# Kernel optimization log

Hardware: AMD Instinct MI355X
Metric: run time of the kernel (lower is better)

## Reference

```python
import jax, jax.numpy as jnp
import numpy as np

DIM = 128
N_IN = DIM * 2 * 6          # 1536
H = N_IN // 2               # 768
W2 = N_IN * 2               # 3072
B, T = 256, 64


def _lrelu(a):
    return jnp.where(a >= 0, a, 0.1 * a)


def _lin(x, w, b):
    # torch Linear: y = x @ w.T + b, w is [out, in]
    return x @ w.T + b


def setup_inputs() -> dict:
    key = jax.random.key(0)
    ks = jax.random.split(key, 32)
    s = 0.02
    d = {
        'x': jax.random.normal(ks[0], (B, T, N_IN), jnp.float32),
        'h0r': jax.random.normal(ks[1], (B, H), jnp.float32) / 100.0,
        'h0i': jax.random.normal(ks[2], (B, H), jnp.float32) / 100.0,
        'Ur_w': jax.random.normal(ks[3], (H, H)) * s, 'Ur_b': jnp.zeros((H,)),
        'Ui_w': jax.random.normal(ks[4], (H, H)) * s, 'Ui_b': jnp.zeros((H,)),
        'Wr_w': jax.random.normal(ks[5], (H, H)) * s, 'Wr_b': jnp.zeros((H,)),
        'Wi_w': jax.random.normal(ks[6], (H, H)) * s, 'Wi_b': jnp.zeros((H,)),
        'l1r_w': jax.random.normal(ks[7], (W2, H)) * s, 'l1r_b': jnp.zeros((W2,)),
        'l1i_w': jax.random.normal(ks[8], (W2, H)) * s, 'l1i_b': jnp.zeros((W2,)),
        'l2r_w': jax.random.normal(ks[9], (W2, W2)) * s, 'l2r_b': jnp.zeros((W2,)),
        'l2i_w': jax.random.normal(ks[10], (W2, W2)) * s, 'l2i_b': jnp.zeros((W2,)),
        'l3r_w': jax.random.normal(ks[11], (W2, W2)) * s, 'l3r_b': jnp.zeros((W2,)),
        'l3i_w': jax.random.normal(ks[12], (W2, W2)) * s, 'l3i_b': jnp.zeros((W2,)),
        'l5_w': jax.random.normal(ks[13], (1, 2 * W2)) * s, 'l5_b': jnp.zeros((1,)),
    }
    return {k: v.astype(jnp.float32) for k, v in d.items()}


def reference(x, h0r, h0i, Ur_w, Ur_b, Ui_w, Ui_b, Wr_w, Wr_b, Wi_w, Wi_b,
              l1r_w, l1r_b, l1i_w, l1i_b, l2r_w, l2r_b, l2i_w, l2i_b,
              l3r_w, l3r_b, l3i_w, l3i_b, l5_w, l5_b):
    xr = x[:, :, :H]            # [B,T,H]
    xi = x[:, :, -H:]
    # Precompute the input projections for every timestep (batched GEMM).
    ur_xr = jnp.einsum('bti,oi->bto', xr, Ur_w) + Ur_b
    ur_xi = jnp.einsum('bti,oi->bto', xi, Ur_w) + Ur_b
    ui_xr = jnp.einsum('bti,oi->bto', xr, Ui_w) + Ui_b
    ui_xi = jnp.einsum('bti,oi->bto', xi, Ui_w) + Ui_b
    # scan over time: [T,B,H]
    seq = (jnp.swapaxes(ur_xr, 0, 1), jnp.swapaxes(ur_xi, 0, 1),
           jnp.swapaxes(ui_xr, 0, 1), jnp.swapaxes(ui_xi, 0, 1))

    def step(h, inp):
        hr, hi = h
        urr, uri, uir, uii = inp
        wr_hr = _lin(hr, Wr_w, Wr_b); wr_hi = _lin(hi, Wr_w, Wr_b)
        wi_hr = _lin(hr, Wi_w, Wi_b); wi_hi = _lin(hi, Wi_w, Wi_b)
        ar = wr_hr - wi_hi + urr - uii
        ai = wr_hi + wi_hr + uri + uir
        return (_lrelu(ar), _lrelu(ai)), None

    (hr, hi), _ = jax.lax.scan(step, (h0r, h0i), seq)
    # complex MLP stages
    xr_, xi_ = hr, hi
    xrn = _lrelu(_lin(xr_, l1r_w, l1r_b)) - _lrelu(_lin(xi_, l1i_w, l1i_b))
    xin = _lrelu(_lin(xi_, l1r_w, l1r_b)) + _lrelu(_lin(xr_, l1i_w, l1i_b))
    xr_, xi_ = xrn, xin
    xrn = _lrelu(_lin(xr_, l2r_w, l2r_b)) - _lrelu(_lin(xi_, l2i_w, l2i_b))
    xin = _lrelu(_lin(xi_, l2r_w, l2r_b)) + _lrelu(_lin(xr_, l2i_w, l2i_b))
    xr_, xi_ = xrn, xin
    xrn = _lrelu(_lin(xr_, l3r_w, l3r_b)) - _lrelu(_lin(xi_, l3i_w, l3i_b))
    xin = _lrelu(_lin(xi_, l3r_w, l3r_b)) + _lrelu(_lin(xr_, l3i_w, l3i_b))
    out = _lrelu(_lin(jnp.concatenate([xrn, xin], axis=1), l5_w, l5_b))
    return out  # [B,1]
```

## Files before the change

kernel.cpp:

```cpp
#include <hip/hip_runtime.h>
#include <stdint.h>

typedef _Float16 h8 __attribute__((ext_vector_type(8)));
typedef float f4 __attribute__((ext_vector_type(4)));

#define DEV __device__ __forceinline__

DEV float lrelu(float v){ return v >= 0.f ? v : 0.1f * v; }

DEV void gl_lds16(const void* g, void* l){
  __builtin_amdgcn_global_load_lds(
      (const __attribute__((address_space(1))) void*)g,
      (__attribute__((address_space(3))) void*)l, 16, 0, 0);
}

template<int BM,int BN,int BK,int WR,int WC,int MODE>
__global__ __launch_bounds__(WR*WC*64)
void gemm_bt(const _Float16* __restrict__ A, const _Float16* __restrict__ Bw,
             const float* __restrict__ bias, const _Float16* __restrict__ Cterm,
             _Float16* __restrict__ D, int M, int N, int K)
{
  constexpr int NW  = WR*WC;
  constexpr int WMT = BM/WR, WNT = BN/WC;
  constexpr int MI  = WMT/16, NI = WNT/16;
  constexpr int RPI = 512/BK;
  constexpr int AIS = BM/RPI/NW, BIS = BN/RPI/NW;
  static_assert(AIS*RPI*NW == BM && BIS*RPI*NW == BN, "tile/stage mismatch");

  __shared__ __align__(16) _Float16 As[BM][BK];
  __shared__ __align__(16) _Float16 Bs[BN][BK];

  int wg = blockIdx.x;
  { int q = (int)gridDim.x >> 3; wg = (wg & 7) * q + (wg >> 3); }
  const int nt = N / BN;
  const int m0 = (wg / nt) * BM, n0 = (wg % nt) * BN;

  const int tid = threadIdx.x, w = tid >> 6, lane = tid & 63;
  const int wm = (w / WC) * WMT, wn = (w % WC) * WNT;
  const int lrow = lane / (BK/8), lkb = (lane % (BK/8)) * 8;
  const int fr = lane & 15, fk = (lane >> 4) * 8, rrow = (lane >> 4) * 4;

  f4 acc[MI][NI];
  f4 zero = {0.f, 0.f, 0.f, 0.f};
  #pragma unroll
  for (int i = 0; i < MI; ++i)
    #pragma unroll
    for (int j = 0; j < NI; ++j) acc[i][j] = zero;

  for (int k0 = 0; k0 < K; k0 += BK) {
    __syncthreads();
    #pragma unroll
    for (int i = 0; i < AIS; ++i) {
      const int r0 = (w*AIS + i) * RPI;
      gl_lds16(A + (size_t)(m0 + r0 + lrow)*K + (k0 + lkb), (void*)&As[r0][0]);
    }
    #pragma unroll
    for (int i = 0; i < BIS; ++i) {
      const int r0 = (w*BIS + i) * RPI;
      gl_lds16(Bw + (size_t)(n0 + r0 + lrow)*K + (k0 + lkb), (void*)&Bs[r0][0]);
    }
    __syncthreads();
    #pragma unroll
    for (int kk = 0; kk < BK; kk += 32) {
      h8 af[MI], bf[NI];
      #pragma unroll
      for (int mi = 0; mi < MI; ++mi) af[mi] = *(const h8*)&As[wm + mi*16 + fr][kk + fk];
      #pragma unroll
      for (int ni = 0; ni < NI; ++ni) bf[ni] = *(const h8*)&Bs[wn + ni*16 + fr][kk + fk];
      #pragma unroll
      for (int mi = 0; mi < MI; ++mi)
        #pragma unroll
        for (int ni = 0; ni < NI; ++ni)
          acc[mi][ni] = __builtin_amdgcn_mfma_f32_16x16x32_f16(af[mi], bf[ni], acc[mi][ni], 0, 0, 0);
    }
  }

  #pragma unroll
  for (int mi = 0; mi < MI; ++mi)
    #pragma unroll
    for (int ni = 0; ni < NI; ++ni) {
      const int n = n0 + wn + ni*16 + fr;
      const float bv = bias[n];
      #pragma unroll
      for (int r = 0; r < 4; ++r) {
        const int m = m0 + wm + mi*16 + rrow + r;
        float v = acc[mi][ni][r] + bv;
        if constexpr (MODE == 0) {
          D[(size_t)((m & 63)*256 + (m >> 6)) * N + n] = (_Float16)v;
        } else if constexpr (MODE == 1) {
          v += (float)Cterm[(size_t)m * N + n];
          v = lrelu(v);
          D[(size_t)m * N + n] = (_Float16)v;
        } else {
          v = lrelu(v);
          D[(size_t)m * N + n] = (_Float16)v;
        }
      }
    }
}

__global__ void k_f2h(const float* __restrict__ s, _Float16* __restrict__ d, long n8){
  const long str = (long)gridDim.x * blockDim.x;
  for (long i = (long)blockIdx.x*blockDim.x + threadIdx.x; i < n8; i += str){
    const long e = i*8;
    f4 a = *(const f4*)(s+e), b = *(const f4*)(s+e+4);
    h8 h = {(_Float16)a[0],(_Float16)a[1],(_Float16)a[2],(_Float16)a[3],
            (_Float16)b[0],(_Float16)b[1],(_Float16)b[2],(_Float16)b[3]};
    *(h8*)(d+e) = h;
  }
}

__global__ void k_build_cplx(const float* __restrict__ Ar, const float* __restrict__ Ai,
                             const float* __restrict__ br, const float* __restrict__ bi,
                             _Float16* __restrict__ W, float* __restrict__ bias)
{
  const long n8 = 1536L*1536/8;
  const long str = (long)gridDim.x*blockDim.x;
  const long t0 = (long)blockIdx.x*blockDim.x + threadIdx.x;
  if (t0 < 1536) bias[t0] = (t0 < 768) ? br[t0] - bi[t0] : br[t0-768] + bi[t0-768];
  for (long i = t0; i < n8; i += str){
    const long e = i*8;
    const int n = (int)(e / 1536), k = (int)(e % 1536);
    const float* src; float sg = 1.f;
    if (n < 768) { if (k < 768) src = Ar + (long)n*768 + k; else { src = Ai + (long)n*768 + (k-768); sg = -1.f; } }
    else         { if (k < 768) src = Ai + (long)(n-768)*768 + k; else src = Ar + (long)(n-768)*768 + (k-768); }
    f4 a = *(const f4*)src, b = *(const f4*)(src+4);
    h8 h = {(_Float16)(a[0]*sg),(_Float16)(a[1]*sg),(_Float16)(a[2]*sg),(_Float16)(a[3]*sg),
            (_Float16)(b[0]*sg),(_Float16)(b[1]*sg),(_Float16)(b[2]*sg),(_Float16)(b[3]*sg)};
    *(h8*)(W + e) = h;
  }
}

__global__ void k_build_cat(const float* __restrict__ lr, const float* __restrict__ li,
                            _Float16* __restrict__ W, int Nh, int K)
{
  const long n8 = (long)Nh*2*K/8;
  const long str = (long)gridDim.x*blockDim.x;
  for (long i = (long)blockIdx.x*blockDim.x + threadIdx.x; i < n8; i += str){
    const long e = i*8;
    const int n = (int)(e / K), k = (int)(e % K);
    const float* src = (n < Nh) ? lr + (long)n*K + k : li + (long)(n-Nh)*K + k;
    f4 a = *(const f4*)src, b = *(const f4*)(src+4);
    h8 h = {(_Float16)a[0],(_Float16)a[1],(_Float16)a[2],(_Float16)a[3],
            (_Float16)b[0],(_Float16)b[1],(_Float16)b[2],(_Float16)b[3]};
    *(h8*)(W + e) = h;
  }
}

__global__ void k_cat_bias(const float* __restrict__ brr, const float* __restrict__ bii,
                           float* __restrict__ bias, int Nh){
  const int t = blockIdx.x*blockDim.x + threadIdx.x;
  if (t < 2*Nh) bias[t] = (t < Nh) ? brr[t] : bii[t - Nh];
}

__global__ void k_hinit(const float* __restrict__ h0r, const float* __restrict__ h0i,
                        _Float16* __restrict__ h){
  const long n8 = 256L*1536/8;
  const long str = (long)gridDim.x*blockDim.x;
  for (long i = (long)blockIdx.x*blockDim.x + threadIdx.x; i < n8; i += str){
    const long e = i*8;
    const int b = (int)(e / 1536), j = (int)(e % 1536);
    const float* src = (j < 768) ? h0r + (long)b*768 + j : h0i + (long)b*768 + (j-768);
    f4 a = *(const f4*)src, c = *(const f4*)(src+4);
    h8 h2 = {(_Float16)a[0],(_Float16)a[1],(_Float16)a[2],(_Float16)a[3],
             (_Float16)c[0],(_Float16)c[1],(_Float16)c[2],(_Float16)c[3]};
    *(h8*)(h + e) = h2;
  }
}

__global__ void k_pack(const _Float16* __restrict__ h, _Float16* __restrict__ A2){
  const long n8 = 512L*768/8;
  const long str = (long)gridDim.x*blockDim.x;
  for (long i = (long)blockIdx.x*blockDim.x + threadIdx.x; i < n8; i += str){
    const long e = i*8;
    const int m = (int)(e / 768), k = (int)(e % 768);
    const _Float16* src = (m < 256) ? h + (long)m*1536 + k : h + (long)(m-256)*1536 + 768 + k;
    *(h8*)(A2 + e) = *(const h8*)src;
  }
}

__global__ void k_combine(const _Float16* __restrict__ LC, _Float16* __restrict__ y){
  const long n8 = 256L*3072/8;
  const long str = (long)gridDim.x*blockDim.x;
  for (long i = (long)blockIdx.x*blockDim.x + threadIdx.x; i < n8; i += str){
    const long e = i*8;
    const int b = (int)(e / 3072), j = (int)(e % 3072);
    h8 arr = *(const h8*)(LC + (long)b*6144 + j);
    h8 aii = *(const h8*)(LC + (long)(256+b)*6144 + 3072 + j);
    h8 air = *(const h8*)(LC + (long)(256+b)*6144 + j);
    h8 ari = *(const h8*)(LC + (long)b*6144 + 3072 + j);
    h8 yr, yi;
    #pragma unroll
    for (int t = 0; t < 8; ++t){
      yr[t] = (_Float16)((float)arr[t] - (float)aii[t]);
      yi[t] = (_Float16)((float)air[t] + (float)ari[t]);
    }
    *(h8*)(y + (long)b*3072 + j) = yr;
    *(h8*)(y + (long)(256+b)*3072 + j) = yi;
  }
}

__global__ void k_final(const _Float16* __restrict__ y, const float* __restrict__ w5,
                        const float* __restrict__ b5, float* __restrict__ out){
  const int b = blockIdx.x, tid = threadIdx.x;
  float s = 0.f;
  for (int j = tid; j < 6144; j += 256){
    float v = (j < 3072) ? (float)y[(long)b*3072 + j] : (float)y[(long)(256+b)*3072 + (j-3072)];
    s += v * w5[j];
  }
  #pragma unroll
  for (int off = 32; off; off >>= 1) s += __shfl_down(s, off);
  __shared__ float red[4];
  if ((tid & 63) == 0) red[tid >> 6] = s;
  __syncthreads();
  if (tid == 0){
    float t = red[0] + red[1] + red[2] + red[3] + b5[0];
    out[b] = lrelu(t);
  }
}

extern "C" void kernel_launch(void* const* d_in, const int* in_sizes, int n_in,
                              void* d_out, int out_size, void* d_ws, size_t ws_size,
                              hipStream_t stream)
{
  const float* x    = (const float*)d_in[0];
  const float* h0r  = (const float*)d_in[1];
  const float* h0i  = (const float*)d_in[2];
  const float* Urw  = (const float*)d_in[3];
  const float* Urb  = (const float*)d_in[4];
  const float* Uiw  = (const float*)d_in[5];
  const float* Uib  = (const float*)d_in[6];
  const float* Wrw  = (const float*)d_in[7];
  const float* Wrb  = (const float*)d_in[8];
  const float* Wiw  = (const float*)d_in[9];
  const float* Wib  = (const float*)d_in[10];
  const float* l1rw = (const float*)d_in[11];
  const float* l1rb = (const float*)d_in[12];
  const float* l1iw = (const float*)d_in[13];
  const float* l1ib = (const float*)d_in[14];
  const float* l2rw = (const float*)d_in[15];
  const float* l2rb = (const float*)d_in[16];
  const float* l2iw = (const float*)d_in[17];
  const float* l2ib = (const float*)d_in[18];
  const float* l3rw = (const float*)d_in[19];
  const float* l3rb = (const float*)d_in[20];
  const float* l3iw = (const float*)d_in[21];
  const float* l3ib = (const float*)d_in[22];
  const float* l5w  = (const float*)d_in[23];
  const float* l5b  = (const float*)d_in[24];
  (void)in_sizes; (void)n_in; (void)out_size; (void)ws_size;

  char* p = (char*)d_ws;
  auto alloc = [&](size_t bytes)->char*{ char* r = p; p += (bytes + 255) & ~(size_t)255; return r; };
  _Float16* xh  = (_Float16*)alloc(25165824ull*2);
  _Float16* cb  = (_Float16*)alloc(25165824ull*2);
  _Float16* Wu  = (_Float16*)alloc(2359296ull*2);
  _Float16* Wc  = (_Float16*)alloc(2359296ull*2);
  float*    ub  = (float*)alloc(1536*4);
  float*    cbs = (float*)alloc(1536*4);
  _Float16* B1  = (_Float16*)alloc(4718592ull*2);
  float*    b1  = (float*)alloc(6144*4);
  _Float16* B2  = (_Float16*)alloc(18874368ull*2);
  float*    b2  = (float*)alloc(6144*4);
  _Float16* B3  = (_Float16*)alloc(18874368ull*2);
  float*    b3  = (float*)alloc(6144*4);
  _Float16* hA  = (_Float16*)alloc(393216ull*2);
  _Float16* hB  = (_Float16*)alloc(393216ull*2);
  _Float16* A2  = (_Float16*)alloc(393216ull*2);
  _Float16* LC  = (_Float16*)alloc(3145728ull*2);
  _Float16* yb  = (_Float16*)alloc(1572864ull*2);

  k_f2h<<<dim3(2048), dim3(256), 0, stream>>>(x, xh, 25165824L/8);
  k_build_cplx<<<dim3(1152), dim3(256), 0, stream>>>(Urw, Uiw, Urb, Uib, Wu, ub);
  k_build_cplx<<<dim3(1152), dim3(256), 0, stream>>>(Wrw, Wiw, Wrb, Wib, Wc, cbs);
  k_build_cat<<<dim3(2048), dim3(256), 0, stream>>>(l1rw, l1iw, B1, 3072, 768);
  k_cat_bias<<<dim3(24), dim3(256), 0, stream>>>(l1rb, l1ib, b1, 3072);
  k_build_cat<<<dim3(2048), dim3(256), 0, stream>>>(l2rw, l2iw, B2, 3072, 3072);
  k_cat_bias<<<dim3(24), dim3(256), 0, stream>>>(l2rb, l2ib, b2, 3072);
  k_build_cat<<<dim3(2048), dim3(256), 0, stream>>>(l3rw, l3iw, B3, 3072, 3072);
  k_cat_bias<<<dim3(24), dim3(256), 0, stream>>>(l3rb, l3ib, b3, 3072);
  k_hinit<<<dim3(192), dim3(256), 0, stream>>>(h0r, h0i, hA);

  gemm_bt<128,128,32,2,2,0><<<dim3(1536), dim3(256), 0, stream>>>(
      xh, Wu, ub, nullptr, cb, 16384, 1536, 1536);

  _Float16* hc = hA; _Float16* hn = hB;
  for (int t = 0; t < 64; ++t) {
    gemm_bt<32,128,64,2,2,1><<<dim3(96), dim3(256), 0, stream>>>(
        hc, Wc, cbs, cb + (size_t)t*393216, hn, 256, 1536, 1536);
    _Float16* tmp = hc; hc = hn; hn = tmp;
  }

  k_pack<<<dim3(192), dim3(256), 0, stream>>>(hc, A2);
  gemm_bt<256,128,64,4,2,2><<<dim3(96), dim3(512), 0, stream>>>(
      A2, B1, b1, nullptr, LC, 512, 6144, 768);
  k_combine<<<dim3(384), dim3(256), 0, stream>>>(LC, yb);
  gemm_bt<256,128,64,4,2,2><<<dim3(96), dim3(512), 0, stream>>>(
      yb, B2, b2, nullptr, LC, 512, 6144, 3072);
  k_combine<<<dim3(384), dim3(256), 0, stream>>>(LC, yb);
  gemm_bt<256,128,64,4,2,2><<<dim3(96), dim3(512), 0, stream>>>(
      yb, B3, b3, nullptr, LC, 512, 6144, 3072);
  k_combine<<<dim3(384), dim3(256), 0, stream>>>(LC, yb);

  k_final<<<dim3(256), dim3(256), 0, stream>>>(yb, l5w, l5b, (float*)d_out);
}
```

Baseline: 2.096 ms.

## Replace per-timestep recurrent GEMM launches with persistent cooperative scan kernel

```diff
diff --git a/kernel.cpp b/kernel.cpp
--- a/kernel.cpp
+++ b/kernel.cpp
@@ -87,16 +87,91 @@
         float v = acc[mi][ni][r] + bv;
         if constexpr (MODE == 0) {
           D[(size_t)((m & 63)*256 + (m >> 6)) * N + n] = (_Float16)v;
-        } else if constexpr (MODE == 1) {
-          v += (float)Cterm[(size_t)m * N + n];
-          v = lrelu(v);
-          D[(size_t)m * N + n] = (_Float16)v;
         } else {
           v = lrelu(v);
           D[(size_t)m * N + n] = (_Float16)v;
         }
       }
     }
+  (void)Cterm;
+}
+
+__global__ __launch_bounds__(384, 1)
+void k_scan(const _Float16* __restrict__ Wc, const float* __restrict__ bias,
+            const _Float16* __restrict__ cb, _Float16* __restrict__ hA,
+            _Float16* __restrict__ hB, int* __restrict__ bar)
+{
+  __shared__ __align__(16) _Float16 Bs[48 * 1544];
+
+  const int bid = blockIdx.x;
+  const int g = bid & 7, j = bid >> 3;
+  const int n0 = j * 48, m0 = g * 32;
+  const int tid = threadIdx.x, w = tid >> 6, lane = tid & 63;
+  const int wr = w / 3, wc = w % 3;
+  const int fr = lane & 15, fk = (lane >> 4) * 8, rrow = (lane >> 4) * 4;
+
+  for (int idx = tid; idx < 48 * 192; idx += 384) {
+    const int r = idx / 192, kc = (idx - r * 192) * 8;
+    *(h8*)(&Bs[r * 1544 + kc]) = *(const h8*)(Wc + (size_t)(n0 + r) * 1536 + kc);
+  }
+
+  const int   ncol  = n0 + wc * 16 + fr;
+  const float bv    = bias[ncol];
+  const int   bsrow = (wc * 16 + fr) * 1544 + fk;
+  const int   arowi = m0 + wr * 16 + fr;
+  const int   orow  = m0 + wr * 16 + rrow;
+  int* cnt = bar + g * 32;
+
+  __syncthreads();
+
+  const _Float16* hin = hA;
+  _Float16* hout = hB;
+
+  for (int t = 0; t < 64; ++t) {
+    const _Float16* cp = cb + ((size_t)t * 256 + orow) * 1536 + ncol;
+    const float cv0 = (float)cp[0];
+    const float cv1 = (float)cp[1536];
+    const float cv2 = (float)cp[3072];
+    const float cv3 = (float)cp[4608];
+
+    const _Float16* arow = hin + (size_t)arowi * 1536 + fk;
+    h8 a[8], b[8];
+    #pragma unroll
+    for (int i = 0; i < 8; ++i) {
+      a[i] = *(const h8*)(arow + i * 32);
+      b[i] = *(const h8*)(&Bs[bsrow + i * 32]);
+    }
+    f4 acc = {0.f, 0.f, 0.f, 0.f};
+    #pragma unroll
+    for (int c8 = 0; c8 < 48; c8 += 8) {
+      #pragma unroll
+      for (int i = 0; i < 8; ++i) {
+        acc = __builtin_amdgcn_mfma_f32_16x16x32_f16(a[i], b[i], acc, 0, 0, 0);
+        if (c8 + 8 < 48) {
+          a[i] = *(const h8*)(arow + (c8 + 8 + i) * 32);
+          b[i] = *(const h8*)(&Bs[bsrow + (c8 + 8 + i) * 32]);
+        }
+      }
+    }
+
+    _Float16* op = hout + (size_t)orow * 1536 + ncol;
+    op[0]    = (_Float16)lrelu(acc[0] + bv + cv0);
+    op[1536] = (_Float16)lrelu(acc[1] + bv + cv1);
+    op[3072] = (_Float16)lrelu(acc[2] + bv + cv2);
+    op[4608] = (_Float16)lrelu(acc[3] + bv + cv3);
+
+    __syncthreads();
+    if (tid == 0) {
+      __hip_atomic_fetch_add(cnt, 1, __ATOMIC_RELEASE, __HIP_MEMORY_SCOPE_AGENT);
+      const int target = 32 * (t + 1);
+      while (__hip_atomic_load(cnt, __ATOMIC_RELAXED, __HIP_MEMORY_SCOPE_AGENT) < target)
+        __builtin_amdgcn_s_sleep(2);
+      (void)__hip_atomic_load(cnt, __ATOMIC_ACQUIRE, __HIP_MEMORY_SCOPE_AGENT);
+    }
+    __syncthreads();
+
+    _Float16* tmp = (_Float16*)hin; hin = hout; hout = tmp;
+  }
 }
 
 __global__ void k_f2h(const float* __restrict__ s, _Float16* __restrict__ d, long n8){
@@ -269,6 +344,7 @@
   _Float16* A2  = (_Float16*)alloc(393216ull*2);
   _Float16* LC  = (_Float16*)alloc(3145728ull*2);
   _Float16* yb  = (_Float16*)alloc(1572864ull*2);
+  int*      bar = (int*)alloc(8*32*4);
 
   k_f2h<<<dim3(2048), dim3(256), 0, stream>>>(x, xh, 25165824L/8);
   k_build_cplx<<<dim3(1152), dim3(256), 0, stream>>>(Urw, Uiw, Urb, Uib, Wu, ub);
@@ -281,17 +357,18 @@
   k_cat_bias<<<dim3(24), dim3(256), 0, stream>>>(l3rb, l3ib, b3, 3072);
   k_hinit<<<dim3(192), dim3(256), 0, stream>>>(h0r, h0i, hA);
 
-  gemm_bt<128,128,32,2,2,0><<<dim3(1536), dim3(256), 0, stream>>>(
+  gemm_bt<128,128,64,2,2,0><<<dim3(1536), dim3(256), 0, stream>>>(
       xh, Wu, ub, nullptr, cb, 16384, 1536, 1536);
 
-  _Float16* hc = hA; _Float16* hn = hB;
-  for (int t = 0; t < 64; ++t) {
-    gemm_bt<32,128,64,2,2,1><<<dim3(96), dim3(256), 0, stream>>>(
-        hc, Wc, cbs, cb + (size_t)t*393216, hn, 256, 1536, 1536);
-    _Float16* tmp = hc; hc = hn; hn = tmp;
-  }
-
-  k_pack<<<dim3(192), dim3(256), 0, stream>>>(hc, A2);
+  hipMemsetAsync(bar, 0, 8*32*sizeof(int), stream);
+  {
+    void* args[] = { (void*)&Wc, (void*)&cbs, (void*)&cb,
+                     (void*)&hA, (void*)&hB, (void*)&bar };
+    hipLaunchCooperativeKernel(reinterpret_cast<void*>(&k_scan),
+                               dim3(256), dim3(384), args, 0, stream);
+  }
+
+  k_pack<<<dim3(192), dim3(256), 0, stream>>>(hA, A2);
   gemm_bt<256,128,64,4,2,2><<<dim3(96), dim3(512), 0, stream>>>(
       A2, B1, b1, nullptr, LC, 512, 6144, 768);
   k_combine<<<dim3(384), dim3(256), 0, stream>>>(LC, yb);
```

After: 1.757 ms. 1.19x faster.
